# Kernel optimization log

Measured on AMD Instinct MI355X. Metric: run time of the kernel, lower is better.

## Reference

```python
import jax, jax.numpy as jnp
import numpy as np

B, T, IDIM, HDIM = 16, 512, 80, 512
TEMPER = 10.0


def _windows(key_pad, n_shifts, win):
    idx = jnp.arange(n_shifts)[:, None] + jnp.arange(win)[None, :]
    return key_pad[..., idx]


def setup_inputs() -> dict:
    key = jax.random.key(0)
    k1, k2, k3 = jax.random.split(key, 3)
    x = jax.random.normal(k1, (B, T, IDIM), dtype=jnp.float32)
    y = jax.random.normal(k2, (B, T, IDIM), dtype=jnp.float32)
    # xavier-uniform fc1 weight, zero bias (per initialize())
    limit = float(np.sqrt(6.0 / (IDIM + HDIM)))
    fc1_w = jax.random.uniform(k3, (HDIM, IDIM), jnp.float32, -limit, limit)
    fc1_b = jnp.zeros((HDIM,), jnp.float32)
    return {"x": x, "y": y, "fc1_w": fc1_w, "fc1_b": fc1_b}


def reference(x, y, fc1_w, fc1_b):
    idim = x.shape[-1]
    pad = idim - 1                 # idim_q - 1
    S = 2 * idim - 1               # idim_k + idim_q - 1 shift positions

    # ---- _pad_for_shift: (B,T,S,idim) sliding windows over padded key ----
    key_pad = jnp.pad(x, ((0, 0), (0, 0), (pad, pad)))
    kpt = _windows(key_pad, S, idim)                        # (B,T,S,idim)

    # ---- _simiality: cosine similarity per shift, max over shifts ----
    q = y[..., None, :]                                     # (B,T,1,idim)
    denom = jnp.linalg.norm(q, axis=-1) * jnp.linalg.norm(kpt, axis=-1)
    sim = jnp.sum(q * kpt, axis=-1) / denom                 # (B,T,S)
    sim = jnp.where(jnp.isnan(sim), 0.0, sim)
    sim_max = jnp.max(sim, axis=-1)                         # (B,T)
    sim_max_idx = jnp.argmax(sim, axis=-1)                  # (B,T)

    # ---- select best-shift window (argaug, scale=False, single theta) ----
    x_aug = jnp.take_along_axis(kpt, sim_max_idx[..., None, None], axis=-2)[..., 0, :]  # (B,T,idim)

    # ---- temp_softmax attention (detached in original) ----
    score = x_aug * y
    attn = jax.nn.softmax(score / TEMPER, axis=-1)
    attn = jnp.where(jnp.isnan(attn), 0.0, attn)
    attn = jax.lax.stop_gradient(attn)
    x_attn = x_aug * attn                                   # (B,T,idim)

    # ---- _reverse_pad_for_shift: undo the shift on x_attn ----
    kp2 = jnp.pad(x_attn, ((0, 0), (0, 0), (pad, pad)))
    kpt2 = _windows(kp2, S, idim)                           # (B,T,S,idim)
    rev_idx = 2 * idim - 2 - sim_max_idx                    # p_aug = shift index
    x_ele = jnp.take_along_axis(kpt2, rev_idx[..., None, None], axis=-2)[..., 0, :]

    # ---- fc1 MLP on shifted-attended features ----
    h = jnp.einsum('bti,hi->bth', x_attn, fc1_w) + fc1_b    # (B,T,hdim)
    return h
```

## Files before the change

kernel.cpp:

```cpp
#include <hip/hip_runtime.h>
#include <math.h>

#define BT    8192
#define IDIM  80
#define HDIM  512
#define SPAN  159
#define PADX  320
#define LDK   104

typedef unsigned short ushort_t;
typedef __attribute__((ext_vector_type(8))) short short8;
typedef __attribute__((ext_vector_type(4))) float floatx4;
typedef __attribute__((ext_vector_type(4))) unsigned short ushort4v;

__device__ inline ushort_t f2bf(float f) {
    union { float f; unsigned int i; } v; v.f = f;
    unsigned int x = v.i;
    return (ushort_t)((x + 0x7fffu + ((x >> 16) & 1u)) >> 16);
}

__global__ __launch_bounds__(256) void k_attn(const float* __restrict__ x,
                                              const float* __restrict__ y,
                                              ushort_t* __restrict__ xattn) {
    __shared__ float xp[4][PADX];
    __shared__ float ysm[4][IDIM];
    const int w    = threadIdx.x >> 6;
    const int lane = threadIdx.x & 63;
    const int row  = blockIdx.x * 4 + w;
    const float* xr = x + (size_t)row * IDIM;
    const float* yr = y + (size_t)row * IDIM;

    for (int j = lane; j < PADX; j += 64) xp[w][j] = 0.f;
    __syncthreads();
    float yy = 0.f;
    if (lane < 20) {
        float4 xv = *(const float4*)(xr + lane * 4);
        float4 yv = *(const float4*)(yr + lane * 4);
        int b = 79 + lane * 4;
        xp[w][b + 0] = xv.x; xp[w][b + 1] = xv.y;
        xp[w][b + 2] = xv.z; xp[w][b + 3] = xv.w;
        int c = lane * 4;
        ysm[w][c + 0] = yv.x; ysm[w][c + 1] = yv.y;
        ysm[w][c + 2] = yv.z; ysm[w][c + 3] = yv.w;
        yy = yv.x * yv.x + yv.y * yv.y + yv.z * yv.z + yv.w * yv.w;
    }
    __syncthreads();
    #pragma unroll
    for (int off = 32; off; off >>= 1) yy += __shfl_xor(yy, off);

    const float* xpw = xp[w];
    const float* ysw = ysm[w];
    float d0 = 0.f, d1 = 0.f, d2 = 0.f, n0 = 0.f, n1 = 0.f, n2 = 0.f;
    #pragma unroll 4
    for (int i = 0; i < IDIM; ++i) {
        float yv = ysw[i];
        float a0 = xpw[lane + i];
        float a1 = xpw[lane + 64 + i];
        float a2 = xpw[lane + 128 + i];
        d0 += yv * a0; n0 += a0 * a0;
        d1 += yv * a1; n1 += a1 * a1;
        d2 += yv * a2; n2 += a2 * a2;
    }
    float s0 = (n0 > 0.f) ? d0 / sqrtf(yy * n0) : 0.f;
    float s1 = (n1 > 0.f) ? d1 / sqrtf(yy * n1) : 0.f;
    float s2 = (lane < 31) ? ((n2 > 0.f) ? d2 / sqrtf(yy * n2) : 0.f) : -INFINITY;

    float bv = s0; int bi = lane;
    if (s1 > bv) { bv = s1; bi = lane + 64; }
    if (s2 > bv) { bv = s2; bi = lane + 128; }
    #pragma unroll
    for (int off = 32; off; off >>= 1) {
        float ov = __shfl_xor(bv, off);
        int   oi = __shfl_xor(bi, off);
        if (ov > bv || (ov == bv && oi < bi)) { bv = ov; bi = oi; }
    }

    float xa0 = xpw[bi + lane];
    float yv0 = ysw[lane];
    float z0  = (xa0 * yv0) / 10.0f;
    float xa1 = 0.f, z1 = -INFINITY;
    if (lane < 16) {
        xa1 = xpw[bi + lane + 64];
        float yv1 = ysw[lane + 64];
        z1 = (xa1 * yv1) / 10.0f;
    }
    float m = fmaxf(z0, z1);
    #pragma unroll
    for (int off = 32; off; off >>= 1) m = fmaxf(m, __shfl_xor(m, off));
    float e0 = expf(z0 - m);
    float e1 = (lane < 16) ? expf(z1 - m) : 0.f;
    float es = e0 + e1;
    #pragma unroll
    for (int off = 32; off; off >>= 1) es += __shfl_xor(es, off);
    float inv = 1.0f / es;

    ushort_t* orow = xattn + (size_t)row * IDIM;
    orow[lane] = f2bf(xa0 * (e0 * inv));
    if (lane < 16) orow[lane + 64] = f2bf(xa1 * (e1 * inv));
}

__global__ __launch_bounds__(256) void k_gemm_mfma(const ushort_t* __restrict__ xattn,
                                                   const float* __restrict__ wmat,
                                                   const float* __restrict__ bias,
                                                   float* __restrict__ out) {
    __shared__ __align__(16) ushort_t Abf[64][LDK];
    __shared__ __align__(16) ushort_t Wbf[64][LDK];
    const int tid = threadIdx.x;
    const int rb  = blockIdx.x * 64;
    const int cb  = blockIdx.y * 64;

    if (tid < 64) {
        ushort4v z = {0, 0, 0, 0};
        *(ushort4v*)&Abf[tid][80] = z; *(ushort4v*)&Abf[tid][84] = z;
        *(ushort4v*)&Abf[tid][88] = z; *(ushort4v*)&Abf[tid][92] = z;
        *(ushort4v*)&Wbf[tid][80] = z; *(ushort4v*)&Wbf[tid][84] = z;
        *(ushort4v*)&Wbf[tid][88] = z; *(ushort4v*)&Wbf[tid][92] = z;
    }
    #pragma unroll
    for (int q = 0; q < 3; ++q) {
        int idx = q * 256 + tid;
        if (idx < 640) {
            int r  = idx / 10;
            int kp = (idx % 10) * 8;
            uint4 v = *(const uint4*)(xattn + (size_t)(rb + r) * IDIM + kp);
            *(uint4*)&Abf[r][kp] = v;
        }
    }
    #pragma unroll
    for (int q = 0; q < 5; ++q) {
        int idx = q * 256 + tid;
        int r   = idx / 20;
        int kp  = (idx % 20) * 4;
        float4 wv = *(const float4*)(wmat + (size_t)(cb + r) * IDIM + kp);
        ushort4v wb = { f2bf(wv.x), f2bf(wv.y), f2bf(wv.z), f2bf(wv.w) };
        *(ushort4v*)&Wbf[r][kp] = wb;
    }
    __syncthreads();

    const int wv   = tid >> 6;
    const int lane = tid & 63;
    const int m    = lane & 15;
    const int q4   = lane >> 4;

    short8 af[3];
    #pragma unroll
    for (int kt = 0; kt < 3; ++kt)
        af[kt] = *(const short8*)&Abf[16 * wv + m][q4 * 8 + kt * 32];

    floatx4 acc[4] = {{0.f,0.f,0.f,0.f}, {0.f,0.f,0.f,0.f},
                      {0.f,0.f,0.f,0.f}, {0.f,0.f,0.f,0.f}};
    #pragma unroll
    for (int ct = 0; ct < 4; ++ct) {
        #pragma unroll
        for (int kt = 0; kt < 3; ++kt) {
            short8 bf = *(const short8*)&Wbf[ct * 16 + m][q4 * 8 + kt * 32];
            acc[ct] = __builtin_amdgcn_mfma_f32_16x16x32_bf16(af[kt], bf, acc[ct], 0, 0, 0);
        }
    }

    #pragma unroll
    for (int ct = 0; ct < 4; ++ct) {
        int col = cb + ct * 16 + m;
        float bsv = bias[col];
        int row0 = rb + 16 * wv + q4 * 4;
        #pragma unroll
        for (int i = 0; i < 4; ++i)
            out[(size_t)(row0 + i) * HDIM + col] = acc[ct][i] + bsv;
    }
}

extern "C" void kernel_launch(void* const* d_in, const int* in_sizes, int n_in,
                              void* d_out, int out_size, void* d_ws, size_t ws_size,
                              hipStream_t stream) {
    const float* x  = (const float*)d_in[0];
    const float* y  = (const float*)d_in[1];
    const float* wm = (const float*)d_in[2];
    const float* bs = (const float*)d_in[3];
    float* out = (float*)d_out;
    ushort_t* xattn = (ushort_t*)d_ws;

    k_attn<<<dim3(BT / 4), 256, 0, stream>>>(x, y, xattn);
    k_gemm_mfma<<<dim3(BT / 64, HDIM / 64), 256, 0, stream>>>(xattn, wm, bs, out);
}
```

Baseline: 84.14 us.

## Fuse attention and fc1 GEMM into one kernel with block-resident weights

Merges the shift-attention kernel and the MFMA GEMM into one kernel. Each 512-thread block processes 32 rows, writes the bf16 attended features straight to LDS, then multiplies them against the full bf16-converted fc1 weight held in LDS. This removes the intermediate global round trip and the second launch. In exchange every block reconverts the whole 512x80 weight matrix. With only 256 blocks at one block per CU, occupancy is low and the attention phase runs one row at a time with barriers between rows. The similarity loop also now broadcasts y values with readlane instead of reading them from LDS.

```diff
diff --git a/kernel.cpp b/kernel.cpp
--- a/kernel.cpp
+++ b/kernel.cpp
@@ -7,6 +7,8 @@
 #define SPAN  159
 #define PADX  320
 #define LDK   104
+#define RPB   32
+#define NBLK  (BT / RPB)
 
 typedef unsigned short ushort_t;
 typedef __attribute__((ext_vector_type(8))) short short8;
@@ -19,150 +21,159 @@
     return (ushort_t)((x + 0x7fffu + ((x >> 16) & 1u)) >> 16);
 }
 
-__global__ __launch_bounds__(256) void k_attn(const float* __restrict__ x,
-                                              const float* __restrict__ y,
-                                              ushort_t* __restrict__ xattn) {
-    __shared__ float xp[4][PADX];
-    __shared__ float ysm[4][IDIM];
-    const int w    = threadIdx.x >> 6;
-    const int lane = threadIdx.x & 63;
-    const int row  = blockIdx.x * 4 + w;
-    const float* xr = x + (size_t)row * IDIM;
-    const float* yr = y + (size_t)row * IDIM;
+__device__ inline float rlane(float v, int l) {
+    return __uint_as_float((unsigned int)__builtin_amdgcn_readlane((int)__float_as_uint(v), l));
+}
 
-    for (int j = lane; j < PADX; j += 64) xp[w][j] = 0.f;
-    __syncthreads();
-    float yy = 0.f;
-    if (lane < 20) {
-        float4 xv = *(const float4*)(xr + lane * 4);
-        float4 yv = *(const float4*)(yr + lane * 4);
-        int b = 79 + lane * 4;
-        xp[w][b + 0] = xv.x; xp[w][b + 1] = xv.y;
-        xp[w][b + 2] = xv.z; xp[w][b + 3] = xv.w;
-        int c = lane * 4;
-        ysm[w][c + 0] = yv.x; ysm[w][c + 1] = yv.y;
-        ysm[w][c + 2] = yv.z; ysm[w][c + 3] = yv.w;
-        yy = yv.x * yv.x + yv.y * yv.y + yv.z * yv.z + yv.w * yv.w;
-    }
-    __syncthreads();
+__global__ __launch_bounds__(512, 1) void k_fused(const float* __restrict__ x,
+                                                  const float* __restrict__ y,
+                                                  const float* __restrict__ wmat,
+                                                  const float* __restrict__ bias,
+                                                  float* __restrict__ out) {
+    __shared__ __align__(16) ushort_t Wbf[HDIM][LDK];
+    __shared__ __align__(16) ushort_t Abf[RPB][LDK];
+
+    const int tid  = threadIdx.x;
+    const int wv   = tid >> 6;
+    const int lane = tid & 63;
+    const int rb   = blockIdx.x * RPB;
+
+    float* scratch = (float*)(void*)&Wbf[0][0];
+    float* xpw = scratch + wv * PADX;
+    float* ysw = scratch + 8 * PADX + wv * IDIM;
+
+    for (int j = lane; j < PADX; j += 64) xpw[j] = 0.f;
+
+    float4 xbuf[4], ybuf[4];
     #pragma unroll
-    for (int off = 32; off; off >>= 1) yy += __shfl_xor(yy, off);
-
-    const float* xpw = xp[w];
-    const float* ysw = ysm[w];
-    float d0 = 0.f, d1 = 0.f, d2 = 0.f, n0 = 0.f, n1 = 0.f, n2 = 0.f;
-    #pragma unroll 4
-    for (int i = 0; i < IDIM; ++i) {
-        float yv = ysw[i];
-        float a0 = xpw[lane + i];
-        float a1 = xpw[lane + 64 + i];
-        float a2 = xpw[lane + 128 + i];
-        d0 += yv * a0; n0 += a0 * a0;
-        d1 += yv * a1; n1 += a1 * a1;
-        d2 += yv * a2; n2 += a2 * a2;
-    }
-    float s0 = (n0 > 0.f) ? d0 / sqrtf(yy * n0) : 0.f;
-    float s1 = (n1 > 0.f) ? d1 / sqrtf(yy * n1) : 0.f;
-    float s2 = (lane < 31) ? ((n2 > 0.f) ? d2 / sqrtf(yy * n2) : 0.f) : -INFINITY;
-
-    float bv = s0; int bi = lane;
-    if (s1 > bv) { bv = s1; bi = lane + 64; }
-    if (s2 > bv) { bv = s2; bi = lane + 128; }
-    #pragma unroll
-    for (int off = 32; off; off >>= 1) {
-        float ov = __shfl_xor(bv, off);
-        int   oi = __shfl_xor(bi, off);
-        if (ov > bv || (ov == bv && oi < bi)) { bv = ov; bi = oi; }
+    for (int r = 0; r < 4; ++r) {
+        const int row = rb + wv * 4 + r;
+        if (lane < 20) {
+            xbuf[r] = *(const float4*)(x + (size_t)row * IDIM + lane * 4);
+            ybuf[r] = *(const float4*)(y + (size_t)row * IDIM + lane * 4);
+        }
     }
 
-    float xa0 = xpw[bi + lane];
-    float yv0 = ysw[lane];
-    float z0  = (xa0 * yv0) / 10.0f;
-    float xa1 = 0.f, z1 = -INFINITY;
-    if (lane < 16) {
-        xa1 = xpw[bi + lane + 64];
-        float yv1 = ysw[lane + 64];
-        z1 = (xa1 * yv1) / 10.0f;
+    for (int r = 0; r < 4; ++r) {
+        const int lrow = wv * 4 + r;
+        float4 yv4 = ybuf[r];
+        float yy = 0.f;
+        if (lane < 20) {
+            float4 xv = xbuf[r];
+            int b = 79 + lane * 4;
+            xpw[b + 0] = xv.x; xpw[b + 1] = xv.y;
+            xpw[b + 2] = xv.z; xpw[b + 3] = xv.w;
+            int c = lane * 4;
+            ysw[c + 0] = yv4.x; ysw[c + 1] = yv4.y;
+            ysw[c + 2] = yv4.z; ysw[c + 3] = yv4.w;
+            yy = yv4.x * yv4.x + yv4.y * yv4.y + yv4.z * yv4.z + yv4.w * yv4.w;
+        }
+        __syncthreads();
+        #pragma unroll
+        for (int off = 32; off; off >>= 1) yy += __shfl_xor(yy, off);
+
+        float d0 = 0.f, d1 = 0.f, d2 = 0.f, n0 = 0.f, n1 = 0.f, n2 = 0.f;
+        #pragma unroll 4
+        for (int i4 = 0; i4 < 20; ++i4) {
+            float yv0 = rlane(yv4.x, i4);
+            float yv1 = rlane(yv4.y, i4);
+            float yv2 = rlane(yv4.z, i4);
+            float yv3 = rlane(yv4.w, i4);
+            const float* p = xpw + lane + i4 * 4;
+            float a00 = p[0],   a01 = p[1],   a02 = p[2],   a03 = p[3];
+            float a10 = p[64],  a11 = p[65],  a12 = p[66],  a13 = p[67];
+            float a20 = p[128], a21 = p[129], a22 = p[130], a23 = p[131];
+            d0 = fmaf(yv3, a03, fmaf(yv2, a02, fmaf(yv1, a01, fmaf(yv0, a00, d0))));
+            n0 = fmaf(a03, a03, fmaf(a02, a02, fmaf(a01, a01, fmaf(a00, a00, n0))));
+            d1 = fmaf(yv3, a13, fmaf(yv2, a12, fmaf(yv1, a11, fmaf(yv0, a10, d1))));
+            n1 = fmaf(a13, a13, fmaf(a12, a12, fmaf(a11, a11, fmaf(a10, a10, n1))));
+            d2 = fmaf(yv3, a23, fmaf(yv2, a22, fmaf(yv1, a21, fmaf(yv0, a20, d2))));
+            n2 = fmaf(a23, a23, fmaf(a22, a22, fmaf(a21, a21, fmaf(a20, a20, n2))));
+        }
+        float s0 = (n0 > 0.f) ? d0 / sqrtf(yy * n0) : 0.f;
+        float s1 = (n1 > 0.f) ? d1 / sqrtf(yy * n1) : 0.f;
+        float s2 = (lane < 31) ? ((n2 > 0.f) ? d2 / sqrtf(yy * n2) : 0.f) : -INFINITY;
+
+        float bv = s0; int bi = lane;
+        if (s1 > bv) { bv = s1; bi = lane + 64; }
+        if (s2 > bv) { bv = s2; bi = lane + 128; }
+        #pragma unroll
+        for (int off = 32; off; off >>= 1) {
+            float ov = __shfl_xor(bv, off);
+            int   oi = __shfl_xor(bi, off);
+            if (ov > bv || (ov == bv && oi < bi)) { bv = ov; bi = oi; }
+        }
+
+        float xa0 = xpw[bi + lane];
+        float yv0 = ysw[lane];
+        float z0  = (xa0 * yv0) / 10.0f;
+        float xa1 = 0.f, z1 = -INFINITY;
+        if (lane < 16) {
+            xa1 = xpw[bi + lane + 64];
+            float yv1 = ysw[lane + 64];
+            z1 = (xa1 * yv1) / 10.0f;
+        }
+        float m = fmaxf(z0, z1);
+        #pragma unroll
+        for (int off = 32; off; off >>= 1) m = fmaxf(m, __shfl_xor(m, off));
+        float e0 = expf(z0 - m);
+        float e1 = (lane < 16) ? expf(z1 - m) : 0.f;
+        float es = e0 + e1;
+        #pragma unroll
+        for (int off = 32; off; off >>= 1) es += __shfl_xor(es, off);
+        float inv = 1.0f / es;
+
+        Abf[lrow][lane] = f2bf(xa0 * (e0 * inv));
+        ushort_t a64 = 0;
+        if (lane < 16) a64 = f2bf(xa1 * (e1 * inv));
+        if (lane < 32) Abf[lrow][lane + 64] = a64;
+        __syncthreads();
     }
-    float m = fmaxf(z0, z1);
+
     #pragma unroll
-    for (int off = 32; off; off >>= 1) m = fmaxf(m, __shfl_xor(m, off));
-    float e0 = expf(z0 - m);
-    float e1 = (lane < 16) ? expf(z1 - m) : 0.f;
-    float es = e0 + e1;
-    #pragma unroll
-    for (int off = 32; off; off >>= 1) es += __shfl_xor(es, off);
-    float inv = 1.0f / es;
-
-    ushort_t* orow = xattn + (size_t)row * IDIM;
-    orow[lane] = f2bf(xa0 * (e0 * inv));
-    if (lane < 16) orow[lane + 64] = f2bf(xa1 * (e1 * inv));
-}
-
-__global__ __launch_bounds__(256) void k_gemm_mfma(const ushort_t* __restrict__ xattn,
-                                                   const float* __restrict__ wmat,
-                                                   const float* __restrict__ bias,
-                                                   float* __restrict__ out) {
-    __shared__ __align__(16) ushort_t Abf[64][LDK];
-    __shared__ __align__(16) ushort_t Wbf[64][LDK];
-    const int tid = threadIdx.x;
-    const int rb  = blockIdx.x * 64;
-    const int cb  = blockIdx.y * 64;
-
-    if (tid < 64) {
+    for (int q = 0; q < 20; ++q) {
+        int idx = q * 512 + tid;
+        int r   = idx / 20;
+        int kp  = (idx % 20) * 4;
+        float4 wv4 = *(const float4*)(wmat + (size_t)r * IDIM + kp);
+        ushort4v wb = { f2bf(wv4.x), f2bf(wv4.y), f2bf(wv4.z), f2bf(wv4.w) };
+        *(ushort4v*)&Wbf[r][kp] = wb;
+    }
+    {
         ushort4v z = {0, 0, 0, 0};
-        *(ushort4v*)&Abf[tid][80] = z; *(ushort4v*)&Abf[tid][84] = z;
-        *(ushort4v*)&Abf[tid][88] = z; *(ushort4v*)&Abf[tid][92] = z;
         *(ushort4v*)&Wbf[tid][80] = z; *(ushort4v*)&Wbf[tid][84] = z;
         *(ushort4v*)&Wbf[tid][88] = z; *(ushort4v*)&Wbf[tid][92] = z;
     }
-    #pragma unroll
-    for (int q = 0; q < 3; ++q) {
-        int idx = q * 256 + tid;
-        if (idx < 640) {
-            int r  = idx / 10;
-            int kp = (idx % 10) * 8;
-            uint4 v = *(const uint4*)(xattn + (size_t)(rb + r) * IDIM + kp);
-            *(uint4*)&Abf[r][kp] = v;
-        }
-    }
-    #pragma unroll
-    for (int q = 0; q < 5; ++q) {
-        int idx = q * 256 + tid;
-        int r   = idx / 20;
-        int kp  = (idx % 20) * 4;
-        float4 wv = *(const float4*)(wmat + (size_t)(cb + r) * IDIM + kp);
-        ushort4v wb = { f2bf(wv.x), f2bf(wv.y), f2bf(wv.z), f2bf(wv.w) };
-        *(ushort4v*)&Wbf[r][kp] = wb;
-    }
     __syncthreads();
 
-    const int wv   = tid >> 6;
-    const int lane = tid & 63;
+    const int rg   = wv & 1;
+    const int cg   = wv >> 1;
     const int m    = lane & 15;
     const int q4   = lane >> 4;
 
     short8 af[3];
     #pragma unroll
     for (int kt = 0; kt < 3; ++kt)
-        af[kt] = *(const short8*)&Abf[16 * wv + m][q4 * 8 + kt * 32];
+        af[kt] = *(const short8*)&Abf[16 * rg + m][q4 * 8 + kt * 32];
 
-    floatx4 acc[4] = {{0.f,0.f,0.f,0.f}, {0.f,0.f,0.f,0.f},
-                      {0.f,0.f,0.f,0.f}, {0.f,0.f,0.f,0.f}};
+    floatx4 acc[8];
     #pragma unroll
-    for (int ct = 0; ct < 4; ++ct) {
+    for (int ct = 0; ct < 8; ++ct) acc[ct] = (floatx4){0.f, 0.f, 0.f, 0.f};
+
+    #pragma unroll
+    for (int ct = 0; ct < 8; ++ct) {
         #pragma unroll
         for (int kt = 0; kt < 3; ++kt) {
-            short8 bf = *(const short8*)&Wbf[ct * 16 + m][q4 * 8 + kt * 32];
+            short8 bf = *(const short8*)&Wbf[cg * 128 + ct * 16 + m][q4 * 8 + kt * 32];
             acc[ct] = __builtin_amdgcn_mfma_f32_16x16x32_bf16(af[kt], bf, acc[ct], 0, 0, 0);
         }
     }
 
     #pragma unroll
-    for (int ct = 0; ct < 4; ++ct) {
-        int col = cb + ct * 16 + m;
+    for (int ct = 0; ct < 8; ++ct) {
+        int col = cg * 128 + ct * 16 + m;
         float bsv = bias[col];
-        int row0 = rb + 16 * wv + q4 * 4;
+        int row0 = rb + 16 * rg + q4 * 4;
         #pragma unroll
         for (int i = 0; i < 4; ++i)
             out[(size_t)(row0 + i) * HDIM + col] = acc[ct][i] + bsv;
@@ -177,8 +188,7 @@
     const float* wm = (const float*)d_in[2];
     const float* bs = (const float*)d_in[3];
     float* out = (float*)d_out;
-    ushort_t* xattn = (ushort_t*)d_ws;
+    (void)d_ws; (void)ws_size;
 
-    k_attn<<<dim3(BT / 4), 256, 0, stream>>>(x, y, xattn);
-    k_gemm_mfma<<<dim3(BT / 64, HDIM / 64), 256, 0, stream>>>(xattn, wm, bs, out);
+    k_fused<<<dim3(NBLK), 512, 0, stream>>>(x, y, wm, bs, out);
 }
```

Result: slower. 93.49 us (+11.1%).

## Register-block shift similarity: four contiguous shifts per lane, broadcast y via readlane

Applied to the files above, without the earlier changes.

Each lane now computes four adjacent shift positions instead of three strided ones. It reads the padded key as float4 from shared memory with a rolling register window, and broadcasts query values with readlane instead of shared-memory loads. This cuts LDS traffic per FMA in the similarity loop and removes one barrier by shrinking the padded buffer. In exchange it raises register pressure and uses a different accumulation order.

```diff
diff --git a/kernel.cpp b/kernel.cpp
--- a/kernel.cpp
+++ b/kernel.cpp
@@ -5,7 +5,7 @@
 #define IDIM  80
 #define HDIM  512
 #define SPAN  159
-#define PADX  320
+#define SXQ   84
 #define LDK   104
 
 typedef unsigned short ushort_t;
@@ -19,55 +19,80 @@
     return (ushort_t)((x + 0x7fffu + ((x >> 16) & 1u)) >> 16);
 }
 
+__device__ inline float rlane(float v, int l) {
+    return __uint_as_float((unsigned int)__builtin_amdgcn_readlane((int)__float_as_uint(v), l));
+}
+
 __global__ __launch_bounds__(256) void k_attn(const float* __restrict__ x,
                                               const float* __restrict__ y,
                                               ushort_t* __restrict__ xattn) {
-    __shared__ float xp[4][PADX];
+    __shared__ __align__(16) float sx[4][SXQ * 4];
     __shared__ float ysm[4][IDIM];
     const int w    = threadIdx.x >> 6;
     const int lane = threadIdx.x & 63;
     const int row  = blockIdx.x * 4 + w;
     const float* xr = x + (size_t)row * IDIM;
     const float* yr = y + (size_t)row * IDIM;
-
-    for (int j = lane; j < PADX; j += 64) xp[w][j] = 0.f;
-    __syncthreads();
+    float* sxw = sx[w];
+
+    {
+        float4 z = make_float4(0.f, 0.f, 0.f, 0.f);
+        *(float4*)&sxw[lane * 4] = z;
+        if (lane < SXQ - 64) *(float4*)&sxw[(lane + 64) * 4] = z;
+    }
+    float4 yv4 = make_float4(0.f, 0.f, 0.f, 0.f);
     float yy = 0.f;
     if (lane < 20) {
         float4 xv = *(const float4*)(xr + lane * 4);
-        float4 yv = *(const float4*)(yr + lane * 4);
+        yv4       = *(const float4*)(yr + lane * 4);
         int b = 79 + lane * 4;
-        xp[w][b + 0] = xv.x; xp[w][b + 1] = xv.y;
-        xp[w][b + 2] = xv.z; xp[w][b + 3] = xv.w;
+        sxw[b + 0] = xv.x; sxw[b + 1] = xv.y;
+        sxw[b + 2] = xv.z; sxw[b + 3] = xv.w;
         int c = lane * 4;
-        ysm[w][c + 0] = yv.x; ysm[w][c + 1] = yv.y;
-        ysm[w][c + 2] = yv.z; ysm[w][c + 3] = yv.w;
-        yy = yv.x * yv.x + yv.y * yv.y + yv.z * yv.z + yv.w * yv.w;
+        ysm[w][c + 0] = yv4.x; ysm[w][c + 1] = yv4.y;
+        ysm[w][c + 2] = yv4.z; ysm[w][c + 3] = yv4.w;
+        yy = yv4.x * yv4.x + yv4.y * yv4.y + yv4.z * yv4.z + yv4.w * yv4.w;
     }
     __syncthreads();
     #pragma unroll
     for (int off = 32; off; off >>= 1) yy += __shfl_xor(yy, off);
 
-    const float* xpw = xp[w];
-    const float* ysw = ysm[w];
-    float d0 = 0.f, d1 = 0.f, d2 = 0.f, n0 = 0.f, n1 = 0.f, n2 = 0.f;
-    #pragma unroll 4
-    for (int i = 0; i < IDIM; ++i) {
-        float yv = ysw[i];
-        float a0 = xpw[lane + i];
-        float a1 = xpw[lane + 64 + i];
-        float a2 = xpw[lane + 128 + i];
-        d0 += yv * a0; n0 += a0 * a0;
-        d1 += yv * a1; n1 += a1 * a1;
-        d2 += yv * a2; n2 += a2 * a2;
-    }
+    float d0 = 0.f, d1 = 0.f, d2 = 0.f, d3 = 0.f;
+    float n0 = 0.f, n1 = 0.f, n2 = 0.f, n3 = 0.f;
+    float4 cur = *(const float4*)&sxw[4 * lane];
+    #pragma unroll
+    for (int i4 = 0; i4 < 20; ++i4) {
+        float4 nxt = *(const float4*)&sxw[4 * (lane + i4 + 1)];
+        float y0 = rlane(yv4.x, i4);
+        float y1 = rlane(yv4.y, i4);
+        float y2 = rlane(yv4.z, i4);
+        float y3 = rlane(yv4.w, i4);
+        float v0 = cur.x, v1 = cur.y, v2 = cur.z, v3 = cur.w;
+        float v4 = nxt.x, v5 = nxt.y, v6 = nxt.z;
+        d0 = fmaf(y3, v3, fmaf(y2, v2, fmaf(y1, v1, fmaf(y0, v0, d0))));
+        d1 = fmaf(y3, v4, fmaf(y2, v3, fmaf(y1, v2, fmaf(y0, v1, d1))));
+        d2 = fmaf(y3, v5, fmaf(y2, v4, fmaf(y1, v3, fmaf(y0, v2, d2))));
+        d3 = fmaf(y3, v6, fmaf(y2, v5, fmaf(y1, v4, fmaf(y0, v3, d3))));
+        n0 = fmaf(v3, v3, fmaf(v2, v2, fmaf(v1, v1, fmaf(v0, v0, n0))));
+        n1 = fmaf(v4, v4, fmaf(v3, v3, fmaf(v2, v2, fmaf(v1, v1, n1))));
+        n2 = fmaf(v5, v5, fmaf(v4, v4, fmaf(v3, v3, fmaf(v2, v2, n2))));
+        n3 = fmaf(v6, v6, fmaf(v5, v5, fmaf(v4, v4, fmaf(v3, v3, n3))));
+        cur = nxt;
+    }
+    const int sbase = 4 * lane;
     float s0 = (n0 > 0.f) ? d0 / sqrtf(yy * n0) : 0.f;
     float s1 = (n1 > 0.f) ? d1 / sqrtf(yy * n1) : 0.f;
-    float s2 = (lane < 31) ? ((n2 > 0.f) ? d2 / sqrtf(yy * n2) : 0.f) : -INFINITY;
-
-    float bv = s0; int bi = lane;
-    if (s1 > bv) { bv = s1; bi = lane + 64; }
-    if (s2 > bv) { bv = s2; bi = lane + 128; }
+    float s2 = (n2 > 0.f) ? d2 / sqrtf(yy * n2) : 0.f;
+    float s3 = (n3 > 0.f) ? d3 / sqrtf(yy * n3) : 0.f;
+    if (sbase + 0 > SPAN - 1) s0 = -INFINITY;
+    if (sbase + 1 > SPAN - 1) s1 = -INFINITY;
+    if (sbase + 2 > SPAN - 1) s2 = -INFINITY;
+    if (sbase + 3 > SPAN - 1) s3 = -INFINITY;
+
+    float bv = s0; int bi = sbase;
+    if (s1 > bv) { bv = s1; bi = sbase + 1; }
+    if (s2 > bv) { bv = s2; bi = sbase + 2; }
+    if (s3 > bv) { bv = s3; bi = sbase + 3; }
     #pragma unroll
     for (int off = 32; off; off >>= 1) {
         float ov = __shfl_xor(bv, off);
@@ -75,12 +100,13 @@
         if (ov > bv || (ov == bv && oi < bi)) { bv = ov; bi = oi; }
     }
 
-    float xa0 = xpw[bi + lane];
+    const float* ysw = ysm[w];
+    float xa0 = sxw[bi + lane];
     float yv0 = ysw[lane];
     float z0  = (xa0 * yv0) / 10.0f;
     float xa1 = 0.f, z1 = -INFINITY;
     if (lane < 16) {
-        xa1 = xpw[bi + lane + 64];
+        xa1 = sxw[bi + lane + 64];
         float yv1 = ysw[lane + 64];
         z1 = (xa1 * yv1) / 10.0f;
     }
```

Result: no change. 84.12 us (-0.0%).
